# Optimization experiments

Hardware: AMD Instinct MI355X
Metric: run time of the kernel (lower is better)

## Reference

```python
import jax, jax.numpy as jnp
import numpy as np

C = 768
R = 16
H = C // R  # 48


def setup_inputs() -> dict:
    key = jax.random.key(0)
    ks = jax.random.split(key, 5)
    x = jax.random.normal(ks[0], (32, 64, 64, C), dtype=jnp.float32)
    # Xavier-uniform linear weights (stored as [in, out] for jnp.dot)
    lim1 = float(np.sqrt(6.0 / (C + H)))
    W1 = jax.random.uniform(ks[1], (C, H), dtype=jnp.float32, minval=-lim1, maxval=lim1)
    b1 = jax.random.normal(ks[2], (H,), dtype=jnp.float32) * 1e-6
    lim2 = float(np.sqrt(6.0 / (H + C)))
    W2 = jax.random.uniform(ks[3], (H, C), dtype=jnp.float32, minval=-lim2, maxval=lim2)
    b2 = jax.random.normal(ks[4], (C,), dtype=jnp.float32) * 1e-6
    gamma = jnp.ones((C,), dtype=jnp.float32)
    beta = jnp.zeros((C,), dtype=jnp.float32)
    return {"x": x, "W1": W1, "b1": b1, "W2": W2, "b2": b2, "gamma": gamma, "beta": beta}


def _layernorm(x, gamma, beta, eps=1e-5):
    mu = jnp.mean(x, axis=-1, keepdims=True)
    var = jnp.mean(jnp.square(x - mu), axis=-1, keepdims=True)
    return (x - mu) * jax.lax.rsqrt(var + eps) * gamma + beta


def reference(x, W1, b1, W2, b2, gamma, beta):
    # x: [b, h, w, c]; LayerNorm over c, bottleneck MLP, residual add.
    out1 = _layernorm(x, gamma, beta)
    hid = out1 @ W1 + b1                       # [b,h,w,H]
    hid = hid * jax.nn.sigmoid(1.702 * hid)    # QuickGELU
    out = hid @ W2 + b2                        # [b,h,w,c]
    return x + out
```

## Files before the change

kernel.cpp:

```cpp
#include <hip/hip_runtime.h>
#include <hip/hip_bf16.h>
#include <stdint.h>

#define CDIM 768
#define HDIM 48

typedef float  f32x4  __attribute__((ext_vector_type(4)));
typedef short  bf16x8 __attribute__((ext_vector_type(8)));
typedef unsigned short u16x4 __attribute__((ext_vector_type(4)));

__device__ __forceinline__ unsigned short f2bf(float x) {
    __hip_bfloat16 h = __float2bfloat16(x);
    return *reinterpret_cast<unsigned short*>(&h);
}
__device__ __forceinline__ float b2f(short s) {
    union { float f; uint32_t u; } v;
    v.u = ((uint32_t)(unsigned short)s) << 16;
    return v.f;
}
#define SB0() __builtin_amdgcn_sched_barrier(0)

__global__ __launch_bounds__(256) void prep_kernel(
    const float* __restrict__ W1, const float* __restrict__ b1,
    const float* __restrict__ W2,
    const float* __restrict__ gamma, const float* __restrict__ beta,
    unsigned short* __restrict__ w1p, unsigned short* __restrict__ w2p,
    float* __restrict__ b1p, float* __restrict__ cs1)
{
    const int blk = blockIdx.x, tid = threadIdx.x;
    const int l = tid & 63;
    if (blk < 18) {
        const int fid = blk * 4 + (tid >> 6);
        const int kt = fid / 3, nt = fid % 3;
        const int k0 = kt * 32 + 8 * (l >> 4);
        const int n  = nt * 16 + (l & 15);
        bf16x8 v;
        #pragma unroll
        for (int b = 0; b < 8; ++b) {
            const int k = k0 + b;
            v[b] = (short)f2bf(gamma[k] * W1[k * HDIM + n]);
        }
        *reinterpret_cast<bf16x8*>(w1p + (size_t)(fid * 64 + l) * 8) = v;
    } else if (blk < 42) {
        const int fid = (blk - 18) * 4 + (tid >> 6);
        const int kt = fid / 48, nt = fid % 48;
        const int k0 = kt * 32 + 8 * (l >> 4);
        const int n  = nt * 16 + (l & 15);
        bf16x8 v;
        #pragma unroll
        for (int b = 0; b < 8; ++b) {
            const int k = k0 + b;
            const float w = (k < HDIM) ? W2[k * CDIM + n] : 0.0f;
            v[b] = (short)f2bf(w);
        }
        *reinterpret_cast<bf16x8*>(w2p + (size_t)(fid * 64 + l) * 8) = v;
    } else {
        const int j = tid >> 2, p = tid & 3;
        float sb = 0.f, sg = 0.f;
        if (j < HDIM) {
            for (int c = p * 192; c < (p + 1) * 192; ++c) {
                const float w = W1[c * HDIM + j];
                sb += beta[c]  * w;
                sg += gamma[c] * w;
            }
        }
        sb += __shfl_xor(sb, 1); sb += __shfl_xor(sb, 2);
        sg += __shfl_xor(sg, 1); sg += __shfl_xor(sg, 2);
        if (p == 0 && j < HDIM) { b1p[j] = b1[j] + sb; cs1[j] = sg; }
    }
}

__global__ __launch_bounds__(256, 2) void mlp_kernel(
    const float* __restrict__ x,
    const float* __restrict__ b2g,
    const unsigned short* __restrict__ w1p,
    const unsigned short* __restrict__ w2p,
    const float* __restrict__ b1p,
    const float* __restrict__ cs1,
    float* __restrict__ out)
{
    __shared__ __align__(16) char  lds_buf[4][16896];
    __shared__ __align__(16) float lds_b2[CDIM];
    __shared__ __align__(16) float lds_b1[HDIM];
    __shared__ __align__(16) float lds_cs[HDIM];

    const int tid  = threadIdx.x;
    const int w    = tid >> 6;
    const int l    = tid & 63;
    const int lrow = l & 15;
    const int lg   = l >> 4;

    if (tid < 192)       reinterpret_cast<f32x4*>(lds_b2)[tid]       = reinterpret_cast<const f32x4*>(b2g)[tid];
    else if (tid < 204)  reinterpret_cast<f32x4*>(lds_b1)[tid - 192] = reinterpret_cast<const f32x4*>(b1p)[tid - 192];
    else if (tid < 216)  reinterpret_cast<f32x4*>(lds_cs)[tid - 204] = reinterpret_cast<const f32x4*>(cs1)[tid - 204];
    __syncthreads();

    char* const wb = lds_buf[w];
    const size_t m0 = ((size_t)blockIdx.x * 4 + w) * 16;
    const char* const xg = (const char*)x + m0 * 3072;

    const bf16x8* __restrict__ w1f = reinterpret_cast<const bf16x8*>(w1p);
    const bf16x8* __restrict__ w2f = reinterpret_cast<const bf16x8*>(w2p);

    {
        f32x4 xv[16];
        #pragma unroll
        for (int r = 0; r < 16; ++r)
            xv[r] = *reinterpret_cast<const f32x4*>(xg + r * 3072 + l * 16);
        #pragma unroll
        for (int r = 0; r < 16; ++r) {
            u16x4 pk;
            #pragma unroll
            for (int e = 0; e < 4; ++e) pk[e] = f2bf(xv[r][e]);
            *reinterpret_cast<u16x4*>(wb + r * 528 + l * 8) = pk;
        }
    }

    f32x4 acc1[3];
    #pragma unroll
    for (int nt = 0; nt < 3; ++nt) { acc1[nt][0]=0.f; acc1[nt][1]=0.f; acc1[nt][2]=0.f; acc1[nt][3]=0.f; }
    float rs = 0.f, rq = 0.f;

    #pragma unroll 1
    for (int j = 0; j < 3; ++j) {
        bf16x8 w1v[24];
        #pragma unroll
        for (int q = 0; q < 24; ++q) w1v[q] = w1f[(j * 24 + q) * 64 + l];
        f32x4 xn[16];
        if (j < 2) {
            #pragma unroll
            for (int r = 0; r < 16; ++r)
                xn[r] = *reinterpret_cast<const f32x4*>(xg + r * 3072 + (j + 1) * 1024 + l * 16);
        }
        SB0();
        const char* bb = wb + (j & 1) * 8448;
        #pragma unroll
        for (int ktl = 0; ktl < 8; ++ktl) {
            const bf16x8 xf = *reinterpret_cast<const bf16x8*>(bb + lrow * 528 + ktl * 64 + lg * 16);
            #pragma unroll
            for (int e = 0; e < 8; ++e) { const float xe = b2f(xf[e]); rs += xe; rq += xe * xe; }
            acc1[0] = __builtin_amdgcn_mfma_f32_16x16x32_bf16(w1v[ktl*3+0], xf, acc1[0], 0, 0, 0);
            acc1[1] = __builtin_amdgcn_mfma_f32_16x16x32_bf16(w1v[ktl*3+1], xf, acc1[1], 0, 0, 0);
            acc1[2] = __builtin_amdgcn_mfma_f32_16x16x32_bf16(w1v[ktl*3+2], xf, acc1[2], 0, 0, 0);
        }
        if (j < 2) {
            #pragma unroll
            for (int r = 0; r < 16; ++r) {
                u16x4 pk;
                #pragma unroll
                for (int e = 0; e < 4; ++e) pk[e] = f2bf(xn[r][e]);
                *reinterpret_cast<u16x4*>(wb + ((j + 1) & 1) * 8448 + r * 528 + l * 8) = pk;
            }
        }
    }

    rs += __shfl_xor(rs, 16); rs += __shfl_xor(rs, 32);
    rq += __shfl_xor(rq, 16); rq += __shfl_xor(rq, 32);
    const float mu   = rs * (1.f / 768.f);
    const float var  = rq * (1.f / 768.f) - mu * mu;
    const float rstd = rsqrtf(var + 1e-5f);

    unsigned short* const hid = reinterpret_cast<unsigned short*>(wb);
    *reinterpret_cast<unsigned long long*>(hid + (l >> 2) * 72 + 48 + (l & 3) * 4) = 0ull;
    #pragma unroll
    for (int nt = 0; nt < 3; ++nt) {
        const int c4 = nt * 16 + 4 * lg;
        const f32x4 bb = *reinterpret_cast<const f32x4*>(&lds_b1[c4]);
        const f32x4 cs = *reinterpret_cast<const f32x4*>(&lds_cs[c4]);
        u16x4 pk;
        #pragma unroll
        for (int r = 0; r < 4; ++r) {
            const float h = rstd * (acc1[nt][r] - mu * cs[r]) + bb[r];
            const float g = h / (1.f + __expf(-1.702f * h));
            pk[r] = f2bf(g);
        }
        *reinterpret_cast<u16x4*>(hid + lrow * 72 + c4) = pk;
    }
    const bf16x8 a2_0 = *reinterpret_cast<const bf16x8*>(hid + lrow * 72 + 8 * lg);
    const bf16x8 a2_1 = *reinterpret_cast<const bf16x8*>(hid + lrow * 72 + 8 * lg + 32);

    const float* __restrict__ xres = x + (m0 + lrow) * CDIM;
    #pragma unroll 1
    for (int t3 = 0; t3 < 3; ++t3) {
        f32x4 res[16];
        #pragma unroll
        for (int i = 0; i < 16; ++i)
            res[i] = *reinterpret_cast<const f32x4*>(xres + (t3 * 16 + i) * 16 + 4 * lg);
        #pragma unroll
        for (int i = 0; i < 16; ++i) {
            const int ct = t3 * 16 + i;
            f32x4 a = {0.f, 0.f, 0.f, 0.f};
            a = __builtin_amdgcn_mfma_f32_16x16x32_bf16(w2f[ct * 64 + l],        a2_0, a, 0, 0, 0);
            a = __builtin_amdgcn_mfma_f32_16x16x32_bf16(w2f[(48 + ct) * 64 + l], a2_1, a, 0, 0, 0);
            const f32x4 bb = *reinterpret_cast<const f32x4*>(&lds_b2[ct * 16 + 4 * lg]);
            f32x4 o;
            #pragma unroll
            for (int r = 0; r < 4; ++r) o[r] = a[r] + bb[r] + res[i][r];
            *reinterpret_cast<f32x4*>(wb + lrow * 1040 + (i * 16 + 4 * lg) * 4) = o;
        }
        #pragma unroll
        for (int r = 0; r < 16; ++r) {
            const f32x4 v = *reinterpret_cast<const f32x4*>(wb + r * 1040 + l * 16);
            *reinterpret_cast<f32x4*>((char*)out + (m0 + r) * 3072 + t3 * 1024 + l * 16) = v;
        }
    }
}

extern "C" void kernel_launch(void* const* d_in, const int* in_sizes, int n_in,
                              void* d_out, int out_size, void* d_ws, size_t ws_size,
                              hipStream_t stream)
{
    const float* x     = (const float*)d_in[0];
    const float* W1    = (const float*)d_in[1];
    const float* b1    = (const float*)d_in[2];
    const float* W2    = (const float*)d_in[3];
    const float* b2    = (const float*)d_in[4];
    const float* gamma = (const float*)d_in[5];
    const float* beta  = (const float*)d_in[6];
    float* out = (float*)d_out;

    unsigned short* w1p = (unsigned short*)d_ws;
    unsigned short* w2p = w1p + 24 * 3 * 64 * 8;
    float* b1p = (float*)(w2p + 2 * 48 * 64 * 8);
    float* cs1 = b1p + 64;

    const int M = in_sizes[0] / CDIM;
    const int blocks = M / 64;

    prep_kernel<<<dim3(43), dim3(256), 0, stream>>>(W1, b1, W2, gamma, beta, w1p, w2p, b1p, cs1);
    mlp_kernel<<<dim3(blocks), dim3(256), 0, stream>>>(x, b2, w1p, w2p, b1p, cs1, out);
}
```

Baseline: 228.3 us.

## Make MLP kernel persistent, overlapping next tile's GEMM1 with current tile's GEMM2

Each wave now handles four 16-row tiles in a grid-stride loop, with a quarter as many blocks launched. While computing the second GEMM and writing output for the current tile, it loads and converts the next tile's input and runs its first GEMM and LayerNorm statistics in the same chunked loop. The goal is to hide global-memory latency across stages, since the kernel is bandwidth bound. In exchange, register pressure rises (launch bounds drop to one block per SIMD group), LDS is split into separate input and output buffers, and the tile count must divide evenly by four.

```diff
diff --git a/kernel.cpp b/kernel.cpp
--- a/kernel.cpp
+++ b/kernel.cpp
@@ -70,7 +70,7 @@
     }
 }
 
-__global__ __launch_bounds__(256, 2) void mlp_kernel(
+__global__ __launch_bounds__(256, 1) void mlp_kernel(
     const float* __restrict__ x,
     const float* __restrict__ b2g,
     const unsigned short* __restrict__ w1p,
@@ -79,7 +79,8 @@
     const float* __restrict__ cs1,
     float* __restrict__ out)
 {
-    __shared__ __align__(16) char  lds_buf[4][16896];
+    __shared__ __align__(16) char  lds_xb[4][8448];
+    __shared__ __align__(16) char  lds_ob[4][16640];
     __shared__ __align__(16) float lds_b2[CDIM];
     __shared__ __align__(16) float lds_b1[HDIM];
     __shared__ __align__(16) float lds_cs[HDIM];
@@ -95,113 +96,228 @@
     else if (tid < 216)  reinterpret_cast<f32x4*>(lds_cs)[tid - 204] = reinterpret_cast<const f32x4*>(cs1)[tid - 204];
     __syncthreads();
 
-    char* const wb = lds_buf[w];
-    const size_t m0 = ((size_t)blockIdx.x * 4 + w) * 16;
-    const char* const xg = (const char*)x + m0 * 3072;
-
+    char* const xb = lds_xb[w];
+    char* const ob = lds_ob[w];
     const bf16x8* __restrict__ w1f = reinterpret_cast<const bf16x8*>(w1p);
     const bf16x8* __restrict__ w2f = reinterpret_cast<const bf16x8*>(w2p);
 
+    const int waveId  = blockIdx.x * 4 + w;
+    const int wstride = gridDim.x * 4;
+
+    int tcur = waveId;
+    f32x4 acc1[3];
+    float rs, rq;
+    bf16x8 a2_0, a2_1;
+
     {
-        f32x4 xv[16];
-        #pragma unroll
-        for (int r = 0; r < 16; ++r)
-            xv[r] = *reinterpret_cast<const f32x4*>(xg + r * 3072 + l * 16);
-        #pragma unroll
-        for (int r = 0; r < 16; ++r) {
-            u16x4 pk;
-            #pragma unroll
-            for (int e = 0; e < 4; ++e) pk[e] = f2bf(xv[r][e]);
-            *reinterpret_cast<u16x4*>(wb + r * 528 + l * 8) = pk;
-        }
-    }
-
-    f32x4 acc1[3];
-    #pragma unroll
-    for (int nt = 0; nt < 3; ++nt) { acc1[nt][0]=0.f; acc1[nt][1]=0.f; acc1[nt][2]=0.f; acc1[nt][3]=0.f; }
-    float rs = 0.f, rq = 0.f;
-
-    #pragma unroll 1
-    for (int j = 0; j < 3; ++j) {
-        bf16x8 w1v[24];
-        #pragma unroll
-        for (int q = 0; q < 24; ++q) w1v[q] = w1f[(j * 24 + q) * 64 + l];
-        f32x4 xn[16];
-        if (j < 2) {
+        const char* const xg = (const char*)x + (size_t)tcur * 16 * 3072;
+        #pragma unroll
+        for (int nt = 0; nt < 3; ++nt) { acc1[nt][0]=0.f; acc1[nt][1]=0.f; acc1[nt][2]=0.f; acc1[nt][3]=0.f; }
+        rs = 0.f; rq = 0.f;
+        {
+            f32x4 xv[16];
             #pragma unroll
             for (int r = 0; r < 16; ++r)
-                xn[r] = *reinterpret_cast<const f32x4*>(xg + r * 3072 + (j + 1) * 1024 + l * 16);
-        }
-        SB0();
-        const char* bb = wb + (j & 1) * 8448;
-        #pragma unroll
-        for (int ktl = 0; ktl < 8; ++ktl) {
-            const bf16x8 xf = *reinterpret_cast<const bf16x8*>(bb + lrow * 528 + ktl * 64 + lg * 16);
-            #pragma unroll
-            for (int e = 0; e < 8; ++e) { const float xe = b2f(xf[e]); rs += xe; rq += xe * xe; }
-            acc1[0] = __builtin_amdgcn_mfma_f32_16x16x32_bf16(w1v[ktl*3+0], xf, acc1[0], 0, 0, 0);
-            acc1[1] = __builtin_amdgcn_mfma_f32_16x16x32_bf16(w1v[ktl*3+1], xf, acc1[1], 0, 0, 0);
-            acc1[2] = __builtin_amdgcn_mfma_f32_16x16x32_bf16(w1v[ktl*3+2], xf, acc1[2], 0, 0, 0);
-        }
-        if (j < 2) {
+                xv[r] = *reinterpret_cast<const f32x4*>(xg + r * 3072 + l * 16);
             #pragma unroll
             for (int r = 0; r < 16; ++r) {
                 u16x4 pk;
                 #pragma unroll
+                for (int e = 0; e < 4; ++e) pk[e] = f2bf(xv[r][e]);
+                *reinterpret_cast<u16x4*>(xb + r * 528 + l * 8) = pk;
+            }
+        }
+        #pragma unroll 1
+        for (int j = 0; j < 3; ++j) {
+            bf16x8 w1v[24];
+            #pragma unroll
+            for (int q = 0; q < 24; ++q) w1v[q] = w1f[(j * 24 + q) * 64 + l];
+            f32x4 xn[16];
+            if (j < 2) {
+                #pragma unroll
+                for (int r = 0; r < 16; ++r)
+                    xn[r] = *reinterpret_cast<const f32x4*>(xg + r * 3072 + (j + 1) * 1024 + l * 16);
+            }
+            SB0();
+            const char* bb = (j & 1) ? ob : xb;
+            #pragma unroll
+            for (int ktl = 0; ktl < 8; ++ktl) {
+                const bf16x8 xf = *reinterpret_cast<const bf16x8*>(bb + lrow * 528 + ktl * 64 + lg * 16);
+                #pragma unroll
+                for (int e = 0; e < 8; ++e) { const float xe = b2f(xf[e]); rs += xe; rq += xe * xe; }
+                acc1[0] = __builtin_amdgcn_mfma_f32_16x16x32_bf16(w1v[ktl*3+0], xf, acc1[0], 0, 0, 0);
+                acc1[1] = __builtin_amdgcn_mfma_f32_16x16x32_bf16(w1v[ktl*3+1], xf, acc1[1], 0, 0, 0);
+                acc1[2] = __builtin_amdgcn_mfma_f32_16x16x32_bf16(w1v[ktl*3+2], xf, acc1[2], 0, 0, 0);
+            }
+            if (j < 2) {
+                char* nb = ((j + 1) & 1) ? ob : xb;
+                #pragma unroll
+                for (int r = 0; r < 16; ++r) {
+                    u16x4 pk;
+                    #pragma unroll
+                    for (int e = 0; e < 4; ++e) pk[e] = f2bf(xn[r][e]);
+                    *reinterpret_cast<u16x4*>(nb + r * 528 + l * 8) = pk;
+                }
+            }
+        }
+    }
+    {
+        rs += __shfl_xor(rs, 16); rs += __shfl_xor(rs, 32);
+        rq += __shfl_xor(rq, 16); rq += __shfl_xor(rq, 32);
+        const float mu   = rs * (1.f / 768.f);
+        const float var  = rq * (1.f / 768.f) - mu * mu;
+        const float rstd = rsqrtf(var + 1e-5f);
+        unsigned short* const hid = reinterpret_cast<unsigned short*>(xb);
+        *reinterpret_cast<unsigned long long*>(hid + (l >> 2) * 72 + 48 + (l & 3) * 4) = 0ull;
+        #pragma unroll
+        for (int nt = 0; nt < 3; ++nt) {
+            const int c4 = nt * 16 + 4 * lg;
+            const f32x4 bb = *reinterpret_cast<const f32x4*>(&lds_b1[c4]);
+            const f32x4 cs = *reinterpret_cast<const f32x4*>(&lds_cs[c4]);
+            u16x4 pk;
+            #pragma unroll
+            for (int r = 0; r < 4; ++r) {
+                const float h = rstd * (acc1[nt][r] - mu * cs[r]) + bb[r];
+                const float g = h / (1.f + __expf(-1.702f * h));
+                pk[r] = f2bf(g);
+            }
+            *reinterpret_cast<u16x4*>(hid + lrow * 72 + c4) = pk;
+        }
+        a2_0 = *reinterpret_cast<const bf16x8*>(hid + lrow * 72 + 8 * lg);
+        a2_1 = *reinterpret_cast<const bf16x8*>(hid + lrow * 72 + 8 * lg + 32);
+    }
+
+    #pragma unroll 1
+    for (int g = 0; g < 3; ++g) {
+        const int tnext = tcur + wstride;
+        const char* const xgn = (const char*)x + (size_t)tnext * 16 * 3072;
+        const size_t m0c = (size_t)tcur * 16;
+        const float* __restrict__ xres = x + (m0c + lrow) * CDIM;
+
+        #pragma unroll
+        for (int nt = 0; nt < 3; ++nt) { acc1[nt][0]=0.f; acc1[nt][1]=0.f; acc1[nt][2]=0.f; acc1[nt][3]=0.f; }
+        rs = 0.f; rq = 0.f;
+
+        #pragma unroll 1
+        for (int j = 0; j < 3; ++j) {
+            bf16x8 w2v[32];
+            #pragma unroll
+            for (int i = 0; i < 16; ++i) {
+                const int ct = j * 16 + i;
+                w2v[2 * i]     = w2f[ct * 64 + l];
+                w2v[2 * i + 1] = w2f[(48 + ct) * 64 + l];
+            }
+            SB0();
+            f32x4 res[16];
+            #pragma unroll
+            for (int i = 0; i < 16; ++i)
+                res[i] = *reinterpret_cast<const f32x4*>(xres + j * 256 + i * 16 + 4 * lg);
+            SB0();
+            f32x4 xn[16];
+            #pragma unroll
+            for (int r = 0; r < 16; ++r)
+                xn[r] = *reinterpret_cast<const f32x4*>(xgn + r * 3072 + j * 1024 + l * 16);
+            SB0();
+            #pragma unroll
+            for (int i = 0; i < 16; ++i) {
+                const int ct = j * 16 + i;
+                f32x4 a = {0.f, 0.f, 0.f, 0.f};
+                a = __builtin_amdgcn_mfma_f32_16x16x32_bf16(w2v[2 * i],     a2_0, a, 0, 0, 0);
+                a = __builtin_amdgcn_mfma_f32_16x16x32_bf16(w2v[2 * i + 1], a2_1, a, 0, 0, 0);
+                const f32x4 bb = *reinterpret_cast<const f32x4*>(&lds_b2[ct * 16 + 4 * lg]);
+                f32x4 o;
+                #pragma unroll
+                for (int r = 0; r < 4; ++r) o[r] = a[r] + bb[r] + res[i][r];
+                *reinterpret_cast<f32x4*>(ob + lrow * 1040 + (i * 16 + 4 * lg) * 4) = o;
+            }
+            #pragma unroll
+            for (int r = 0; r < 16; ++r) {
+                const f32x4 v = *reinterpret_cast<const f32x4*>(ob + r * 1040 + l * 16);
+                *reinterpret_cast<f32x4*>((char*)out + (m0c + r) * 3072 + j * 1024 + l * 16) = v;
+            }
+            SB0();
+            #pragma unroll
+            for (int r = 0; r < 16; ++r) {
+                u16x4 pk;
+                #pragma unroll
                 for (int e = 0; e < 4; ++e) pk[e] = f2bf(xn[r][e]);
-                *reinterpret_cast<u16x4*>(wb + ((j + 1) & 1) * 8448 + r * 528 + l * 8) = pk;
-            }
-        }
-    }
-
-    rs += __shfl_xor(rs, 16); rs += __shfl_xor(rs, 32);
-    rq += __shfl_xor(rq, 16); rq += __shfl_xor(rq, 32);
-    const float mu   = rs * (1.f / 768.f);
-    const float var  = rq * (1.f / 768.f) - mu * mu;
-    const float rstd = rsqrtf(var + 1e-5f);
-
-    unsigned short* const hid = reinterpret_cast<unsigned short*>(wb);
-    *reinterpret_cast<unsigned long long*>(hid + (l >> 2) * 72 + 48 + (l & 3) * 4) = 0ull;
-    #pragma unroll
-    for (int nt = 0; nt < 3; ++nt) {
-        const int c4 = nt * 16 + 4 * lg;
-        const f32x4 bb = *reinterpret_cast<const f32x4*>(&lds_b1[c4]);
-        const f32x4 cs = *reinterpret_cast<const f32x4*>(&lds_cs[c4]);
-        u16x4 pk;
-        #pragma unroll
-        for (int r = 0; r < 4; ++r) {
-            const float h = rstd * (acc1[nt][r] - mu * cs[r]) + bb[r];
-            const float g = h / (1.f + __expf(-1.702f * h));
-            pk[r] = f2bf(g);
-        }
-        *reinterpret_cast<u16x4*>(hid + lrow * 72 + c4) = pk;
-    }
-    const bf16x8 a2_0 = *reinterpret_cast<const bf16x8*>(hid + lrow * 72 + 8 * lg);
-    const bf16x8 a2_1 = *reinterpret_cast<const bf16x8*>(hid + lrow * 72 + 8 * lg + 32);
-
-    const float* __restrict__ xres = x + (m0 + lrow) * CDIM;
-    #pragma unroll 1
-    for (int t3 = 0; t3 < 3; ++t3) {
-        f32x4 res[16];
-        #pragma unroll
-        for (int i = 0; i < 16; ++i)
-            res[i] = *reinterpret_cast<const f32x4*>(xres + (t3 * 16 + i) * 16 + 4 * lg);
-        #pragma unroll
-        for (int i = 0; i < 16; ++i) {
-            const int ct = t3 * 16 + i;
-            f32x4 a = {0.f, 0.f, 0.f, 0.f};
-            a = __builtin_amdgcn_mfma_f32_16x16x32_bf16(w2f[ct * 64 + l],        a2_0, a, 0, 0, 0);
-            a = __builtin_amdgcn_mfma_f32_16x16x32_bf16(w2f[(48 + ct) * 64 + l], a2_1, a, 0, 0, 0);
-            const f32x4 bb = *reinterpret_cast<const f32x4*>(&lds_b2[ct * 16 + 4 * lg]);
-            f32x4 o;
-            #pragma unroll
-            for (int r = 0; r < 4; ++r) o[r] = a[r] + bb[r] + res[i][r];
-            *reinterpret_cast<f32x4*>(wb + lrow * 1040 + (i * 16 + 4 * lg) * 4) = o;
-        }
-        #pragma unroll
-        for (int r = 0; r < 16; ++r) {
-            const f32x4 v = *reinterpret_cast<const f32x4*>(wb + r * 1040 + l * 16);
-            *reinterpret_cast<f32x4*>((char*)out + (m0 + r) * 3072 + t3 * 1024 + l * 16) = v;
+                *reinterpret_cast<u16x4*>(xb + r * 528 + l * 8) = pk;
+            }
+            bf16x8 w1v[24];
+            #pragma unroll
+            for (int q = 0; q < 24; ++q) w1v[q] = w1f[(j * 24 + q) * 64 + l];
+            #pragma unroll
+            for (int ktl = 0; ktl < 8; ++ktl) {
+                const bf16x8 xf = *reinterpret_cast<const bf16x8*>(xb + lrow * 528 + ktl * 64 + lg * 16);
+                #pragma unroll
+                for (int e = 0; e < 8; ++e) { const float xe = b2f(xf[e]); rs += xe; rq += xe * xe; }
+                acc1[0] = __builtin_amdgcn_mfma_f32_16x16x32_bf16(w1v[ktl*3+0], xf, acc1[0], 0, 0, 0);
+                acc1[1] = __builtin_amdgcn_mfma_f32_16x16x32_bf16(w1v[ktl*3+1], xf, acc1[1], 0, 0, 0);
+                acc1[2] = __builtin_amdgcn_mfma_f32_16x16x32_bf16(w1v[ktl*3+2], xf, acc1[2], 0, 0, 0);
+            }
+        }
+
+        rs += __shfl_xor(rs, 16); rs += __shfl_xor(rs, 32);
+        rq += __shfl_xor(rq, 16); rq += __shfl_xor(rq, 32);
+        const float mu   = rs * (1.f / 768.f);
+        const float var  = rq * (1.f / 768.f) - mu * mu;
+        const float rstd = rsqrtf(var + 1e-5f);
+        unsigned short* const hid = reinterpret_cast<unsigned short*>(xb);
+        *reinterpret_cast<unsigned long long*>(hid + (l >> 2) * 72 + 48 + (l & 3) * 4) = 0ull;
+        #pragma unroll
+        for (int nt = 0; nt < 3; ++nt) {
+            const int c4 = nt * 16 + 4 * lg;
+            const f32x4 bb = *reinterpret_cast<const f32x4*>(&lds_b1[c4]);
+            const f32x4 cs = *reinterpret_cast<const f32x4*>(&lds_cs[c4]);
+            u16x4 pk;
+            #pragma unroll
+            for (int r = 0; r < 4; ++r) {
+                const float h = rstd * (acc1[nt][r] - mu * cs[r]) + bb[r];
+                const float g = h / (1.f + __expf(-1.702f * h));
+                pk[r] = f2bf(g);
+            }
+            *reinterpret_cast<u16x4*>(hid + lrow * 72 + c4) = pk;
+        }
+        a2_0 = *reinterpret_cast<const bf16x8*>(hid + lrow * 72 + 8 * lg);
+        a2_1 = *reinterpret_cast<const bf16x8*>(hid + lrow * 72 + 8 * lg + 32);
+
+        tcur = tnext;
+    }
+
+    {
+        const size_t m0c = (size_t)tcur * 16;
+        const float* __restrict__ xres = x + (m0c + lrow) * CDIM;
+        #pragma unroll 1
+        for (int j = 0; j < 3; ++j) {
+            bf16x8 w2v[32];
+            #pragma unroll
+            for (int i = 0; i < 16; ++i) {
+                const int ct = j * 16 + i;
+                w2v[2 * i]     = w2f[ct * 64 + l];
+                w2v[2 * i + 1] = w2f[(48 + ct) * 64 + l];
+            }
+            f32x4 res[16];
+            #pragma unroll
+            for (int i = 0; i < 16; ++i)
+                res[i] = *reinterpret_cast<const f32x4*>(xres + j * 256 + i * 16 + 4 * lg);
+            SB0();
+            #pragma unroll
+            for (int i = 0; i < 16; ++i) {
+                const int ct = j * 16 + i;
+                f32x4 a = {0.f, 0.f, 0.f, 0.f};
+                a = __builtin_amdgcn_mfma_f32_16x16x32_bf16(w2v[2 * i],     a2_0, a, 0, 0, 0);
+                a = __builtin_amdgcn_mfma_f32_16x16x32_bf16(w2v[2 * i + 1], a2_1, a, 0, 0, 0);
+                const f32x4 bb = *reinterpret_cast<const f32x4*>(&lds_b2[ct * 16 + 4 * lg]);
+                f32x4 o;
+                #pragma unroll
+                for (int r = 0; r < 4; ++r) o[r] = a[r] + bb[r] + res[i][r];
+                *reinterpret_cast<f32x4*>(ob + lrow * 1040 + (i * 16 + 4 * lg) * 4) = o;
+            }
+            #pragma unroll
+            for (int r = 0; r < 16; ++r) {
+                const f32x4 v = *reinterpret_cast<const f32x4*>(ob + r * 1040 + l * 16);
+                *reinterpret_cast<f32x4*>((char*)out + (m0c + r) * 3072 + j * 1024 + l * 16) = v;
+            }
         }
     }
 }
@@ -225,7 +341,7 @@
     float* cs1 = b1p + 64;
 
     const int M = in_sizes[0] / CDIM;
-    const int blocks = M / 64;
+    const int blocks = M / 16 / 4 / 4;
 
     prep_kernel<<<dim3(43), dim3(256), 0, stream>>>(W1, b1, W2, gamma, beta, w1p, w2p, b1p, cs1);
     mlp_kernel<<<dim3(blocks), dim3(256), 0, stream>>>(x, b2, w1p, w2p, b1p, cs1, out);
```

Measured after the change: 229.4 us. No clear change (+0.5%).

## Split MLP kernel into producer/consumer warp pipeline over persistent tiles

Applied to the files above, without the earlier changes.

Restructures the fused MLP kernel into 512-thread blocks in which four waves compute LayerNorm, the first GEMM and QuickGELU for a tile while four other waves run the second GEMM and residual write for the previous tile, handing off the hidden activations through LDS. Each block now processes 8 tiles per wave slot in a software pipeline with block-wide barriers, and the grid shrinks by 8x. Consumer waves also preload W2 fragments into registers before the MFMAs. The aim is to overlap the x-load and GEMM1 phase with the GEMM2 and store phase. In exchange it adds barrier stalls, pipeline fill and drain, lower occupancy (one block per CU), and a grid size that assumes M divides by 512.

```diff
diff --git a/kernel.cpp b/kernel.cpp
--- a/kernel.cpp
+++ b/kernel.cpp
@@ -70,7 +70,7 @@
     }
 }
 
-__global__ __launch_bounds__(256, 2) void mlp_kernel(
+__global__ __launch_bounds__(512, 1) void mlp_kernel(
     const float* __restrict__ x,
     const float* __restrict__ b2g,
     const unsigned short* __restrict__ w1p,
@@ -79,7 +79,9 @@
     const float* __restrict__ cs1,
     float* __restrict__ out)
 {
-    __shared__ __align__(16) char  lds_buf[4][16896];
+    __shared__ __align__(16) char lds_xs[4][16896];
+    __shared__ __align__(16) char lds_ob[4][16640];
+    __shared__ __align__(16) unsigned short lds_hid[4][16][72];
     __shared__ __align__(16) float lds_b2[CDIM];
     __shared__ __align__(16) float lds_b1[HDIM];
     __shared__ __align__(16) float lds_cs[HDIM];
@@ -89,120 +91,144 @@
     const int l    = tid & 63;
     const int lrow = l & 15;
     const int lg   = l >> 4;
+    const int pw   = w & 3;
+    const bool producer = (w < 4);
 
     if (tid < 192)       reinterpret_cast<f32x4*>(lds_b2)[tid]       = reinterpret_cast<const f32x4*>(b2g)[tid];
     else if (tid < 204)  reinterpret_cast<f32x4*>(lds_b1)[tid - 192] = reinterpret_cast<const f32x4*>(b1p)[tid - 192];
     else if (tid < 216)  reinterpret_cast<f32x4*>(lds_cs)[tid - 204] = reinterpret_cast<const f32x4*>(cs1)[tid - 204];
     __syncthreads();
 
-    char* const wb = lds_buf[w];
-    const size_t m0 = ((size_t)blockIdx.x * 4 + w) * 16;
-    const char* const xg = (const char*)x + m0 * 3072;
-
     const bf16x8* __restrict__ w1f = reinterpret_cast<const bf16x8*>(w1p);
     const bf16x8* __restrict__ w2f = reinterpret_cast<const bf16x8*>(w2p);
-
-    {
-        f32x4 xv[16];
-        #pragma unroll
-        for (int r = 0; r < 16; ++r)
-            xv[r] = *reinterpret_cast<const f32x4*>(xg + r * 3072 + l * 16);
-        #pragma unroll
-        for (int r = 0; r < 16; ++r) {
-            u16x4 pk;
-            #pragma unroll
-            for (int e = 0; e < 4; ++e) pk[e] = f2bf(xv[r][e]);
-            *reinterpret_cast<u16x4*>(wb + r * 528 + l * 8) = pk;
-        }
-    }
-
-    f32x4 acc1[3];
-    #pragma unroll
-    for (int nt = 0; nt < 3; ++nt) { acc1[nt][0]=0.f; acc1[nt][1]=0.f; acc1[nt][2]=0.f; acc1[nt][3]=0.f; }
-    float rs = 0.f, rq = 0.f;
+    const int nb = gridDim.x;
 
     #pragma unroll 1
-    for (int j = 0; j < 3; ++j) {
-        bf16x8 w1v[24];
-        #pragma unroll
-        for (int q = 0; q < 24; ++q) w1v[q] = w1f[(j * 24 + q) * 64 + l];
-        f32x4 xn[16];
-        if (j < 2) {
-            #pragma unroll
-            for (int r = 0; r < 16; ++r)
-                xn[r] = *reinterpret_cast<const f32x4*>(xg + r * 3072 + (j + 1) * 1024 + l * 16);
-        }
-        SB0();
-        const char* bb = wb + (j & 1) * 8448;
-        #pragma unroll
-        for (int ktl = 0; ktl < 8; ++ktl) {
-            const bf16x8 xf = *reinterpret_cast<const bf16x8*>(bb + lrow * 528 + ktl * 64 + lg * 16);
-            #pragma unroll
-            for (int e = 0; e < 8; ++e) { const float xe = b2f(xf[e]); rs += xe; rq += xe * xe; }
-            acc1[0] = __builtin_amdgcn_mfma_f32_16x16x32_bf16(w1v[ktl*3+0], xf, acc1[0], 0, 0, 0);
-            acc1[1] = __builtin_amdgcn_mfma_f32_16x16x32_bf16(w1v[ktl*3+1], xf, acc1[1], 0, 0, 0);
-            acc1[2] = __builtin_amdgcn_mfma_f32_16x16x32_bf16(w1v[ktl*3+2], xf, acc1[2], 0, 0, 0);
-        }
-        if (j < 2) {
-            #pragma unroll
-            for (int r = 0; r < 16; ++r) {
-                u16x4 pk;
-                #pragma unroll
-                for (int e = 0; e < 4; ++e) pk[e] = f2bf(xn[r][e]);
-                *reinterpret_cast<u16x4*>(wb + ((j + 1) & 1) * 8448 + r * 528 + l * 8) = pk;
+    for (int r = 0; r < 9; ++r) {
+        bf16x8 a2_0, a2_1;
+        if (!producer && r >= 1) {
+            const unsigned short* hs = &lds_hid[pw][0][0];
+            a2_0 = *reinterpret_cast<const bf16x8*>(hs + lrow * 72 + 8 * lg);
+            a2_1 = *reinterpret_cast<const bf16x8*>(hs + lrow * 72 + 8 * lg + 32);
+        }
+        __syncthreads();
+
+        if (producer) {
+            if (r < 8) {
+                const int t = (r * nb + blockIdx.x) * 4 + pw;
+                char* const xb = lds_xs[pw];
+                const char* const xg = (const char*)x + (size_t)t * 16 * 3072;
+                f32x4 acc1[3];
+                #pragma unroll
+                for (int nt = 0; nt < 3; ++nt) { acc1[nt][0]=0.f; acc1[nt][1]=0.f; acc1[nt][2]=0.f; acc1[nt][3]=0.f; }
+                float rs = 0.f, rq = 0.f;
+                {
+                    f32x4 xv[16];
+                    #pragma unroll
+                    for (int rr = 0; rr < 16; ++rr)
+                        xv[rr] = *reinterpret_cast<const f32x4*>(xg + rr * 3072 + l * 16);
+                    #pragma unroll
+                    for (int rr = 0; rr < 16; ++rr) {
+                        u16x4 pk;
+                        #pragma unroll
+                        for (int e = 0; e < 4; ++e) pk[e] = f2bf(xv[rr][e]);
+                        *reinterpret_cast<u16x4*>(xb + rr * 528 + l * 8) = pk;
+                    }
+                }
+                #pragma unroll 1
+                for (int j = 0; j < 3; ++j) {
+                    bf16x8 w1v[24];
+                    #pragma unroll
+                    for (int q = 0; q < 24; ++q) w1v[q] = w1f[(j * 24 + q) * 64 + l];
+                    f32x4 xn[16];
+                    if (j < 2) {
+                        #pragma unroll
+                        for (int rr = 0; rr < 16; ++rr)
+                            xn[rr] = *reinterpret_cast<const f32x4*>(xg + rr * 3072 + (j + 1) * 1024 + l * 16);
+                    }
+                    SB0();
+                    const char* bb = xb + (j & 1) * 8448;
+                    #pragma unroll
+                    for (int ktl = 0; ktl < 8; ++ktl) {
+                        const bf16x8 xf = *reinterpret_cast<const bf16x8*>(bb + lrow * 528 + ktl * 64 + lg * 16);
+                        #pragma unroll
+                        for (int e = 0; e < 8; ++e) { const float xe = b2f(xf[e]); rs += xe; rq += xe * xe; }
+                        acc1[0] = __builtin_amdgcn_mfma_f32_16x16x32_bf16(w1v[ktl*3+0], xf, acc1[0], 0, 0, 0);
+                        acc1[1] = __builtin_amdgcn_mfma_f32_16x16x32_bf16(w1v[ktl*3+1], xf, acc1[1], 0, 0, 0);
+                        acc1[2] = __builtin_amdgcn_mfma_f32_16x16x32_bf16(w1v[ktl*3+2], xf, acc1[2], 0, 0, 0);
+                    }
+                    if (j < 2) {
+                        char* nb2 = xb + ((j + 1) & 1) * 8448;
+                        #pragma unroll
+                        for (int rr = 0; rr < 16; ++rr) {
+                            u16x4 pk;
+                            #pragma unroll
+                            for (int e = 0; e < 4; ++e) pk[e] = f2bf(xn[rr][e]);
+                            *reinterpret_cast<u16x4*>(nb2 + rr * 528 + l * 8) = pk;
+                        }
+                    }
+                }
+                rs += __shfl_xor(rs, 16); rs += __shfl_xor(rs, 32);
+                rq += __shfl_xor(rq, 16); rq += __shfl_xor(rq, 32);
+                const float mu   = rs * (1.f / 768.f);
+                const float var  = rq * (1.f / 768.f) - mu * mu;
+                const float rstd = rsqrtf(var + 1e-5f);
+                unsigned short* const hs = &lds_hid[pw][0][0];
+                *reinterpret_cast<unsigned long long*>(hs + (l >> 2) * 72 + 48 + (l & 3) * 4) = 0ull;
+                #pragma unroll
+                for (int nt = 0; nt < 3; ++nt) {
+                    const int c4 = nt * 16 + 4 * lg;
+                    const f32x4 bb = *reinterpret_cast<const f32x4*>(&lds_b1[c4]);
+                    const f32x4 cs = *reinterpret_cast<const f32x4*>(&lds_cs[c4]);
+                    u16x4 pk;
+                    #pragma unroll
+                    for (int rr = 0; rr < 4; ++rr) {
+                        const float h = rstd * (acc1[nt][rr] - mu * cs[rr]) + bb[rr];
+                        const float g = h / (1.f + __expf(-1.702f * h));
+                        pk[rr] = f2bf(g);
+                    }
+                    *reinterpret_cast<u16x4*>(hs + lrow * 72 + c4) = pk;
+                }
             }
-        }
-    }
-
-    rs += __shfl_xor(rs, 16); rs += __shfl_xor(rs, 32);
-    rq += __shfl_xor(rq, 16); rq += __shfl_xor(rq, 32);
-    const float mu   = rs * (1.f / 768.f);
-    const float var  = rq * (1.f / 768.f) - mu * mu;
-    const float rstd = rsqrtf(var + 1e-5f);
-
-    unsigned short* const hid = reinterpret_cast<unsigned short*>(wb);
-    *reinterpret_cast<unsigned long long*>(hid + (l >> 2) * 72 + 48 + (l & 3) * 4) = 0ull;
-    #pragma unroll
-    for (int nt = 0; nt < 3; ++nt) {
-        const int c4 = nt * 16 + 4 * lg;
-        const f32x4 bb = *reinterpret_cast<const f32x4*>(&lds_b1[c4]);
-        const f32x4 cs = *reinterpret_cast<const f32x4*>(&lds_cs[c4]);
-        u16x4 pk;
-        #pragma unroll
-        for (int r = 0; r < 4; ++r) {
-            const float h = rstd * (acc1[nt][r] - mu * cs[r]) + bb[r];
-            const float g = h / (1.f + __expf(-1.702f * h));
-            pk[r] = f2bf(g);
-        }
-        *reinterpret_cast<u16x4*>(hid + lrow * 72 + c4) = pk;
-    }
-    const bf16x8 a2_0 = *reinterpret_cast<const bf16x8*>(hid + lrow * 72 + 8 * lg);
-    const bf16x8 a2_1 = *reinterpret_cast<const bf16x8*>(hid + lrow * 72 + 8 * lg + 32);
-
-    const float* __restrict__ xres = x + (m0 + lrow) * CDIM;
-    #pragma unroll 1
-    for (int t3 = 0; t3 < 3; ++t3) {
-        f32x4 res[16];
-        #pragma unroll
-        for (int i = 0; i < 16; ++i)
-            res[i] = *reinterpret_cast<const f32x4*>(xres + (t3 * 16 + i) * 16 + 4 * lg);
-        #pragma unroll
-        for (int i = 0; i < 16; ++i) {
-            const int ct = t3 * 16 + i;
-            f32x4 a = {0.f, 0.f, 0.f, 0.f};
-            a = __builtin_amdgcn_mfma_f32_16x16x32_bf16(w2f[ct * 64 + l],        a2_0, a, 0, 0, 0);
-            a = __builtin_amdgcn_mfma_f32_16x16x32_bf16(w2f[(48 + ct) * 64 + l], a2_1, a, 0, 0, 0);
-            const f32x4 bb = *reinterpret_cast<const f32x4*>(&lds_b2[ct * 16 + 4 * lg]);
-            f32x4 o;
-            #pragma unroll
-            for (int r = 0; r < 4; ++r) o[r] = a[r] + bb[r] + res[i][r];
-            *reinterpret_cast<f32x4*>(wb + lrow * 1040 + (i * 16 + 4 * lg) * 4) = o;
-        }
-        #pragma unroll
-        for (int r = 0; r < 16; ++r) {
-            const f32x4 v = *reinterpret_cast<const f32x4*>(wb + r * 1040 + l * 16);
-            *reinterpret_cast<f32x4*>((char*)out + (m0 + r) * 3072 + t3 * 1024 + l * 16) = v;
-        }
+        } else if (r >= 1) {
+            const int t = ((r - 1) * nb + blockIdx.x) * 4 + pw;
+            char* const ob = lds_ob[pw];
+            const size_t m0 = (size_t)t * 16;
+            const float* __restrict__ xres = x + (m0 + lrow) * CDIM;
+            #pragma unroll 1
+            for (int t3 = 0; t3 < 3; ++t3) {
+                bf16x8 w2v[32];
+                #pragma unroll
+                for (int i = 0; i < 16; ++i) {
+                    const int ct = t3 * 16 + i;
+                    w2v[2 * i]     = w2f[ct * 64 + l];
+                    w2v[2 * i + 1] = w2f[(48 + ct) * 64 + l];
+                }
+                f32x4 res[16];
+                #pragma unroll
+                for (int i = 0; i < 16; ++i)
+                    res[i] = *reinterpret_cast<const f32x4*>(xres + (t3 * 16 + i) * 16 + 4 * lg);
+                SB0();
+                #pragma unroll
+                for (int i = 0; i < 16; ++i) {
+                    const int ct = t3 * 16 + i;
+                    f32x4 a = {0.f, 0.f, 0.f, 0.f};
+                    a = __builtin_amdgcn_mfma_f32_16x16x32_bf16(w2v[2 * i],     a2_0, a, 0, 0, 0);
+                    a = __builtin_amdgcn_mfma_f32_16x16x32_bf16(w2v[2 * i + 1], a2_1, a, 0, 0, 0);
+                    const f32x4 bb = *reinterpret_cast<const f32x4*>(&lds_b2[ct * 16 + 4 * lg]);
+                    f32x4 o;
+                    #pragma unroll
+                    for (int rr = 0; rr < 4; ++rr) o[rr] = a[rr] + bb[rr] + res[i][rr];
+                    *reinterpret_cast<f32x4*>(ob + lrow * 1040 + (i * 16 + 4 * lg) * 4) = o;
+                }
+                #pragma unroll
+                for (int rr = 0; rr < 16; ++rr) {
+                    const f32x4 v = *reinterpret_cast<const f32x4*>(ob + rr * 1040 + l * 16);
+                    *reinterpret_cast<f32x4*>((char*)out + (m0 + rr) * 3072 + t3 * 1024 + l * 16) = v;
+                }
+            }
+        }
+        __syncthreads();
     }
 }
 
@@ -225,8 +251,8 @@
     float* cs1 = b1p + 64;
 
     const int M = in_sizes[0] / CDIM;
-    const int blocks = M / 64;
+    const int blocks = M / 16 / 4 / 8;
 
     prep_kernel<<<dim3(43), dim3(256), 0, stream>>>(W1, b1, W2, gamma, beta, w1p, w2p, b1p, cs1);
-    mlp_kernel<<<dim3(blocks), dim3(256), 0, stream>>>(x, b2, w1p, w2p, b1p, cs1, out);
-}
+    mlp_kernel<<<dim3(blocks), dim3(512), 0, stream>>>(x, b2, w1p, w2p, b1p, cs1, out);
+}
```

After: 260.4 us. +14.0%, slower.
